# Performance work log

Measured on AMD Instinct MI355X. Metric: run time of the kernel, lower is better.

## Reference

```python
import jax, jax.numpy as jnp
from jax import lax
import numpy as np

S, B, I, H, O = 65536, 1, 2, 128, 1


def setup_inputs() -> dict:
    key = jax.random.key(0)
    k1, k2, k3, k4 = jax.random.split(key, 4)
    # xavier_normal-style scales
    s_ih = (2.0 / (4 * H + I)) ** 0.5
    s_hh = (2.0 / (4 * H + H)) ** 0.5
    s_out = (2.0 / (H + O)) ** 0.5
    return {
        "x": jax.random.normal(k1, (S, B, I), jnp.float32),
        "h0": jnp.zeros((1, B, H), jnp.float32),
        "c0": jnp.zeros((1, B, H), jnp.float32),
        "W_ih": jax.random.normal(k2, (4 * H, I), jnp.float32) * s_ih,
        "W_hh": jax.random.normal(k3, (4 * H, H), jnp.float32) * s_hh,
        "b_ih": jnp.zeros((4 * H,), jnp.float32),
        "b_hh": jnp.zeros((4 * H,), jnp.float32),
        "W_out": jax.random.normal(k4, (O, H), jnp.float32) * s_out,
        "b_out": jnp.zeros((O,), jnp.float32),
    }


def reference(x, h0, c0, W_ih, W_hh, b_ih, b_hh, W_out, b_out):
    # Precompute input-to-gate projections for all timesteps: (S, B, 4H)
    xg = jnp.einsum("sbi,gi->sbg", x, W_ih) + b_ih + b_hh

    def step(carry, xg_t):
        h, c = carry  # (B, H) each
        gates = xg_t + h @ W_hh.T  # (B, 4H); PyTorch order i,f,g,o
        i, f, g, o = jnp.split(gates, 4, axis=-1)
        i = jax.nn.sigmoid(i)
        f = jax.nn.sigmoid(f)
        g = jnp.tanh(g)
        o = jax.nn.sigmoid(o)
        c = f * c + i * g
        h = o * jnp.tanh(c)
        return (h, c), h

    (_, _), hs = lax.scan(step, (h0[0], c0[0]), xg)  # hs: (S, B, H)
    out = jnp.tanh(hs.transpose(1, 0, 2))  # (B, S, H), matches permute(1,0,2)
    out = out @ W_out.T + b_out  # (B, S, O)
    return out.reshape(out.shape[0] * out.shape[1], -1)  # (B*S, O)
```

## Files before the change

kernel.cpp:

```cpp
#include <hip/hip_runtime.h>

#define S_LEN 65536
#define HDIM 128
#define NTHR 1024

typedef _Float16 half2_t __attribute__((ext_vector_type(2)));
typedef _Float16 half8_t __attribute__((ext_vector_type(8)));

__device__ __forceinline__ float sigm(float x) {
    return 1.0f / (1.0f + __expf(-x));
}
__device__ __forceinline__ float tanh_fast(float x) {
    return 2.0f / (1.0f + __expf(-2.0f * x)) - 1.0f;
}

__device__ __forceinline__ float dot2(half2_t a, half2_t b, float c) {
#if __has_builtin(__builtin_amdgcn_fdot2)
    return __builtin_amdgcn_fdot2(a, b, c, false);
#else
    return fmaf((float)a.x, (float)b.x, fmaf((float)a.y, (float)b.y, c));
#endif
}

#define H_HI_OFF 144

__global__ __launch_bounds__(NTHR)
__attribute__((amdgpu_waves_per_eu(4, 4)))
void lstm_seq_h(const float* __restrict__ x,
                const float* __restrict__ h0,
                const float* __restrict__ c0,
                const float* __restrict__ W_ih,
                const float* __restrict__ W_hh,
                const float* __restrict__ b_ih,
                const float* __restrict__ b_hh,
                _Float16* __restrict__ h_hist)
{
    __shared__ __align__(16) unsigned char h_raw[2 * H_HI_OFF];
    __shared__ float gates_part[2 * 512];

    const int tid  = threadIdx.x;
    const int j    = tid >> 1;
    const int half = tid & 1;

    const float2* wr2 = (const float2*)(W_hh + j * HDIM + half * 64);
#define WDEF(i) half2_t W##i; { float2 t = wr2[i]; \
        W##i.x = (_Float16)t.x; W##i.y = (_Float16)t.y; } \
        asm volatile("" : "+v"(W##i));
    WDEF(0)  WDEF(1)  WDEF(2)  WDEF(3)  WDEF(4)  WDEF(5)  WDEF(6)  WDEF(7)
    WDEF(8)  WDEF(9)  WDEF(10) WDEF(11) WDEF(12) WDEF(13) WDEF(14) WDEF(15)
    WDEF(16) WDEF(17) WDEF(18) WDEF(19) WDEF(20) WDEF(21) WDEF(22) WDEF(23)
    WDEF(24) WDEF(25) WDEF(26) WDEF(27) WDEF(28) WDEF(29) WDEF(30) WDEF(31)
#undef WDEF

    float wih0 = 0.0f, wih1 = 0.0f, bias = 0.0f;
    if (half == 0) {
        wih0 = W_ih[2 * j + 0];
        wih1 = W_ih[2 * j + 1];
        bias = b_ih[j] + b_hh[j];
    }

    float c = 0.0f;
    _Float16* hw = (_Float16*)(h_raw + ((tid < 64) ? 2 * tid
                                                   : H_HI_OFF + 2 * (tid - 64)));
    if (tid < HDIM) {
        c = c0[tid];
        *hw = (_Float16)h0[tid];
    }
    __syncthreads();

    const float2* xp = (const float2*)x;
    float2 xcur = xp[0];
    const half8_t* hp = (const half8_t*)(h_raw + half * H_HI_OFF);

    #pragma unroll 1
    for (int t = 0; t < S_LEN; ++t) {
        const int tn = (t + 1 < S_LEN) ? (t + 1) : (S_LEN - 1);
        float2 xnext = xp[tn];

        float a0 = fmaf(wih0, xcur.x, fmaf(wih1, xcur.y, bias));
        float a1 = 0.0f, a2 = 0.0f, a3 = 0.0f;

#define CHUNK(cc, w0_, w1_, w2_, w3_) {                         \
        half8_t hv = hp[cc];                                    \
        half2_t p0 = { hv[0], hv[1] };                          \
        half2_t p1 = { hv[2], hv[3] };                          \
        half2_t p2 = { hv[4], hv[5] };                          \
        half2_t p3 = { hv[6], hv[7] };                          \
        a0 = dot2(w0_, p0, a0);                                 \
        a1 = dot2(w1_, p1, a1);                                 \
        a2 = dot2(w2_, p2, a2);                                 \
        a3 = dot2(w3_, p3, a3); }
        CHUNK(0, W0,  W1,  W2,  W3)
        CHUNK(1, W4,  W5,  W6,  W7)
        CHUNK(2, W8,  W9,  W10, W11)
        CHUNK(3, W12, W13, W14, W15)
        CHUNK(4, W16, W17, W18, W19)
        CHUNK(5, W20, W21, W22, W23)
        CHUNK(6, W24, W25, W26, W27)
        CHUNK(7, W28, W29, W30, W31)
#undef CHUNK

        gates_part[half * 512 + j] = (a0 + a1) + (a2 + a3);
        __syncthreads();

        if (tid < HDIM) {
            float gi = sigm(gates_part[tid]           + gates_part[tid + 512]);
            float gf = sigm(gates_part[tid + 128]     + gates_part[tid + 640]);
            float gg = tanh_fast(gates_part[tid + 256] + gates_part[tid + 768]);
            float go = sigm(gates_part[tid + 384]     + gates_part[tid + 896]);
            c = fmaf(gf, c, gi * gg);
            float h = go * tanh_fast(c);
            _Float16 hf = (_Float16)h;
            *hw = hf;
            h_hist[t * HDIM + tid] = hf;
        }
        __syncthreads();

        xcur = xnext;
    }
}

__global__ __launch_bounds__(256)
void out_proj(const _Float16* __restrict__ h_hist,
              const float* __restrict__ W_out,
              const float* __restrict__ b_out,
              float* __restrict__ out)
{
    const int lane  = threadIdx.x & 63;
    const int gwave = (blockIdx.x * 256 + threadIdx.x) >> 6;
    const int nwave = (gridDim.x * 256) >> 6;

    const float wo0 = W_out[2 * lane + 0];
    const float wo1 = W_out[2 * lane + 1];
    const float bout = b_out[0];

    for (int t = gwave; t < S_LEN; t += nwave) {
        half2_t hv = ((const half2_t*)(h_hist + t * HDIM))[lane];
        float p = tanh_fast((float)hv.x) * wo0 + tanh_fast((float)hv.y) * wo1;
        #pragma unroll
        for (int off = 32; off > 0; off >>= 1)
            p += __shfl_xor(p, off, 64);
        if (lane == 0) out[t] = p + bout;
    }
}

__global__ __launch_bounds__(NTHR)
__attribute__((amdgpu_waves_per_eu(4, 4)))
void lstm_seq_full(const float* __restrict__ x,
                   const float* __restrict__ h0,
                   const float* __restrict__ c0,
                   const float* __restrict__ W_ih,
                   const float* __restrict__ W_hh,
                   const float* __restrict__ b_ih,
                   const float* __restrict__ b_hh,
                   const float* __restrict__ W_out,
                   const float* __restrict__ b_out,
                   float* __restrict__ out)
{
    __shared__ __align__(16) unsigned char h_raw[2 * H_HI_OFF];
    __shared__ float gates_part[2 * 512];
    __shared__ float red_sh[2];

    const int tid  = threadIdx.x;
    const int j    = tid >> 1;
    const int half = tid & 1;

    const float2* wr2 = (const float2*)(W_hh + j * HDIM + half * 64);
#define WDEF(i) half2_t W##i; { float2 t = wr2[i]; \
        W##i.x = (_Float16)t.x; W##i.y = (_Float16)t.y; } \
        asm volatile("" : "+v"(W##i));
    WDEF(0)  WDEF(1)  WDEF(2)  WDEF(3)  WDEF(4)  WDEF(5)  WDEF(6)  WDEF(7)
    WDEF(8)  WDEF(9)  WDEF(10) WDEF(11) WDEF(12) WDEF(13) WDEF(14) WDEF(15)
    WDEF(16) WDEF(17) WDEF(18) WDEF(19) WDEF(20) WDEF(21) WDEF(22) WDEF(23)
    WDEF(24) WDEF(25) WDEF(26) WDEF(27) WDEF(28) WDEF(29) WDEF(30) WDEF(31)
#undef WDEF

    float wih0 = 0.0f, wih1 = 0.0f, bias = 0.0f;
    if (half == 0) {
        wih0 = W_ih[2 * j + 0];
        wih1 = W_ih[2 * j + 1];
        bias = b_ih[j] + b_hh[j];
    }

    float c = 0.0f, wout = 0.0f;
    _Float16* hw = (_Float16*)(h_raw + ((tid < 64) ? 2 * tid
                                                   : H_HI_OFF + 2 * (tid - 64)));
    if (tid < HDIM) {
        c = c0[tid];
        wout = W_out[tid];
        *hw = (_Float16)h0[tid];
    }
    const float bout = b_out[0];
    __syncthreads();

    const float2* xp = (const float2*)x;
    float2 xcur = xp[0];
    const half8_t* hp = (const half8_t*)(h_raw + half * H_HI_OFF);

    #pragma unroll 1
    for (int t = 0; t < S_LEN; ++t) {
        const int tn = (t + 1 < S_LEN) ? (t + 1) : (S_LEN - 1);
        float2 xnext = xp[tn];

        float a0 = fmaf(wih0, xcur.x, fmaf(wih1, xcur.y, bias));
        float a1 = 0.0f, a2 = 0.0f, a3 = 0.0f;

#define CHUNK(cc, w0_, w1_, w2_, w3_) {                         \
        half8_t hv = hp[cc];                                    \
        half2_t p0 = { hv[0], hv[1] };                          \
        half2_t p1 = { hv[2], hv[3] };                          \
        half2_t p2 = { hv[4], hv[5] };                          \
        half2_t p3 = { hv[6], hv[7] };                          \
        a0 = dot2(w0_, p0, a0);                                 \
        a1 = dot2(w1_, p1, a1);                                 \
        a2 = dot2(w2_, p2, a2);                                 \
        a3 = dot2(w3_, p3, a3); }
        CHUNK(0, W0,  W1,  W2,  W3)
        CHUNK(1, W4,  W5,  W6,  W7)
        CHUNK(2, W8,  W9,  W10, W11)
        CHUNK(3, W12, W13, W14, W15)
        CHUNK(4, W16, W17, W18, W19)
        CHUNK(5, W20, W21, W22, W23)
        CHUNK(6, W24, W25, W26, W27)
        CHUNK(7, W28, W29, W30, W31)
#undef CHUNK

        gates_part[half * 512 + j] = (a0 + a1) + (a2 + a3);
        __syncthreads();

        if (tid < HDIM) {
            float gi = sigm(gates_part[tid]           + gates_part[tid + 512]);
            float gf = sigm(gates_part[tid + 128]     + gates_part[tid + 640]);
            float gg = tanh_fast(gates_part[tid + 256] + gates_part[tid + 768]);
            float go = sigm(gates_part[tid + 384]     + gates_part[tid + 896]);
            c = fmaf(gf, c, gi * gg);
            float h = go * tanh_fast(c);
            *hw = (_Float16)h;

            float p = tanh_fast(h) * wout;
            #pragma unroll
            for (int off = 32; off > 0; off >>= 1)
                p += __shfl_xor(p, off, 64);
            if ((tid & 63) == 0) red_sh[tid >> 6] = p;
        }
        __syncthreads();

        if (tid == 0) out[t] = red_sh[0] + red_sh[1] + bout;
        xcur = xnext;
    }
}

extern "C" void kernel_launch(void* const* d_in, const int* in_sizes, int n_in,
                              void* d_out, int out_size, void* d_ws, size_t ws_size,
                              hipStream_t stream) {
    const float* x     = (const float*)d_in[0];
    const float* h0    = (const float*)d_in[1];
    const float* c0    = (const float*)d_in[2];
    const float* W_ih  = (const float*)d_in[3];
    const float* W_hh  = (const float*)d_in[4];
    const float* b_ih  = (const float*)d_in[5];
    const float* b_hh  = (const float*)d_in[6];
    const float* W_out = (const float*)d_in[7];
    const float* b_out = (const float*)d_in[8];

    const size_t need = (size_t)S_LEN * HDIM * sizeof(_Float16);
    if (ws_size >= need) {
        _Float16* h_hist = (_Float16*)d_ws;
        lstm_seq_h<<<dim3(1), dim3(NTHR), 0, stream>>>(
            x, h0, c0, W_ih, W_hh, b_ih, b_hh, h_hist);
        out_proj<<<dim3(1024), dim3(256), 0, stream>>>(
            h_hist, W_out, b_out, (float*)d_out);
    } else {
        lstm_seq_full<<<dim3(1), dim3(NTHR), 0, stream>>>(
            x, h0, c0, W_ih, W_hh, b_ih, b_hh, W_out, b_out, (float*)d_out);
    }
}
```

Baseline: 45.95 ms.

## Compute recurrent gate matvec with MFMA 16x16x32 in a 512-thread block

Result: faster. 44.20 ms (-3.8%).

```diff
diff --git a/kernel.cpp b/kernel.cpp
--- a/kernel.cpp
+++ b/kernel.cpp
@@ -2,10 +2,10 @@
 
 #define S_LEN 65536
 #define HDIM 128
-#define NTHR 1024
 
 typedef _Float16 half2_t __attribute__((ext_vector_type(2)));
 typedef _Float16 half8_t __attribute__((ext_vector_type(8)));
+typedef float f32x4 __attribute__((ext_vector_type(4)));
 
 __device__ __forceinline__ float sigm(float x) {
     return 1.0f / (1.0f + __expf(-x));
@@ -13,7 +13,6 @@
 __device__ __forceinline__ float tanh_fast(float x) {
     return 2.0f / (1.0f + __expf(-2.0f * x)) - 1.0f;
 }
-
 __device__ __forceinline__ float dot2(half2_t a, half2_t b, float c) {
 #if __has_builtin(__builtin_amdgcn_fdot2)
     return __builtin_amdgcn_fdot2(a, b, c, false);
@@ -22,21 +21,161 @@
 #endif
 }
 
+__global__ __launch_bounds__(512)
+__attribute__((amdgpu_waves_per_eu(2, 2)))
+void lstm_seq_mfma(const float* __restrict__ x,
+                   const float* __restrict__ h0,
+                   const float* __restrict__ c0,
+                   const float* __restrict__ W_ih,
+                   const float* __restrict__ W_hh,
+                   const float* __restrict__ b_ih,
+                   const float* __restrict__ b_hh,
+                   _Float16* __restrict__ h_hist)
+{
+    __shared__ __align__(16) _Float16 h_sh16[HDIM];
+    __shared__ __align__(16) float gates_sh[4 * HDIM];
+
+    const int tid  = threadIdx.x;
+    const int lane = tid & 63;
+    const int w    = tid >> 6;
+    const int m    = lane & 15;
+    const int quad = lane >> 4;
+
+#define LOAD_AF(i, q) \
+    half8_t af_##i##_##q; { \
+        const float* s_ = W_hh + (size_t)(w * 64 + 16 * (i) + m) * HDIM \
+                               + 32 * (q) + 8 * quad; \
+        af_##i##_##q = (half8_t){ \
+            (_Float16)s_[0], (_Float16)s_[1], (_Float16)s_[2], (_Float16)s_[3], \
+            (_Float16)s_[4], (_Float16)s_[5], (_Float16)s_[6], (_Float16)s_[7] }; \
+        asm volatile("" : "+v"(af_##i##_##q)); }
+    LOAD_AF(0, 0) LOAD_AF(0, 1) LOAD_AF(0, 2) LOAD_AF(0, 3)
+    LOAD_AF(1, 0) LOAD_AF(1, 1) LOAD_AF(1, 2) LOAD_AF(1, 3)
+    LOAD_AF(2, 0) LOAD_AF(2, 1) LOAD_AF(2, 2) LOAD_AF(2, 3)
+    LOAD_AF(3, 0) LOAD_AF(3, 1) LOAD_AF(3, 2) LOAD_AF(3, 3)
+#undef LOAD_AF
+
+    float wi0x = 0.f, wi0y = 0.f, bs0 = 0.f;
+    float wi1x = 0.f, wi1y = 0.f, bs1 = 0.f;
+    float wi2x = 0.f, wi2y = 0.f, bs2 = 0.f;
+    float wi3x = 0.f, wi3y = 0.f, bs3 = 0.f;
+    float c = 0.0f;
+    if (tid < HDIM) {
+        wi0x = W_ih[2 * tid];            wi0y = W_ih[2 * tid + 1];
+        wi1x = W_ih[2 * (tid + 128)];    wi1y = W_ih[2 * (tid + 128) + 1];
+        wi2x = W_ih[2 * (tid + 256)];    wi2y = W_ih[2 * (tid + 256) + 1];
+        wi3x = W_ih[2 * (tid + 384)];    wi3y = W_ih[2 * (tid + 384) + 1];
+        bs0 = b_ih[tid]       + b_hh[tid];
+        bs1 = b_ih[tid + 128] + b_hh[tid + 128];
+        bs2 = b_ih[tid + 256] + b_hh[tid + 256];
+        bs3 = b_ih[tid + 384] + b_hh[tid + 384];
+        c = c0[tid];
+        h_sh16[tid] = (_Float16)h0[tid];
+    }
+    __syncthreads();
+
+    const float2* xp = (const float2*)x;
+    float2 xcur = {0.f, 0.f}, xnext = {0.f, 0.f};
+    if (tid < HDIM) xcur = xp[0];
+
+    half8_t bf0 = (half8_t){0,0,0,0,0,0,0,0};
+    half8_t bf1 = bf0, bf2 = bf0, bf3 = bf0;
+
+    #pragma unroll 1
+    for (int t = 0; t < S_LEN; ++t) {
+        if (m == 0) {
+            const half8_t* hb = (const half8_t*)h_sh16;
+            bf0 = hb[quad];
+            bf1 = hb[4 + quad];
+            bf2 = hb[8 + quad];
+            bf3 = hb[12 + quad];
+        }
+        f32x4 acc0 = {0.f, 0.f, 0.f, 0.f};
+        f32x4 acc1 = {0.f, 0.f, 0.f, 0.f};
+        f32x4 acc2 = {0.f, 0.f, 0.f, 0.f};
+        f32x4 acc3 = {0.f, 0.f, 0.f, 0.f};
+#define MFMA_TILE(i) \
+        acc##i = __builtin_amdgcn_mfma_f32_16x16x32_f16(af_##i##_0, bf0, acc##i, 0, 0, 0); \
+        acc##i = __builtin_amdgcn_mfma_f32_16x16x32_f16(af_##i##_1, bf1, acc##i, 0, 0, 0); \
+        acc##i = __builtin_amdgcn_mfma_f32_16x16x32_f16(af_##i##_2, bf2, acc##i, 0, 0, 0); \
+        acc##i = __builtin_amdgcn_mfma_f32_16x16x32_f16(af_##i##_3, bf3, acc##i, 0, 0, 0);
+        MFMA_TILE(0) MFMA_TILE(1) MFMA_TILE(2) MFMA_TILE(3)
+#undef MFMA_TILE
+        if (m == 0) {
+            f32x4* gp = (f32x4*)gates_sh + w * 16 + quad;
+            gp[0]  = acc0;
+            gp[4]  = acc1;
+            gp[8]  = acc2;
+            gp[12] = acc3;
+        }
+
+        if (tid < HDIM) {
+            const int tn = (t + 1 < S_LEN) ? (t + 1) : (S_LEN - 1);
+            xnext = xp[tn];
+        }
+        __syncthreads();
+
+        if (tid < HDIM) {
+            float gi = sigm(gates_sh[tid]
+                            + fmaf(wi0x, xcur.x, fmaf(wi0y, xcur.y, bs0)));
+            float gf = sigm(gates_sh[tid + 128]
+                            + fmaf(wi1x, xcur.x, fmaf(wi1y, xcur.y, bs1)));
+            float gg = tanh_fast(gates_sh[tid + 256]
+                            + fmaf(wi2x, xcur.x, fmaf(wi2y, xcur.y, bs2)));
+            float go = sigm(gates_sh[tid + 384]
+                            + fmaf(wi3x, xcur.x, fmaf(wi3y, xcur.y, bs3)));
+            c = fmaf(gf, c, gi * gg);
+            float h = go * tanh_fast(c);
+            _Float16 hf = (_Float16)h;
+            h_sh16[tid] = hf;
+            h_hist[t * HDIM + tid] = hf;
+            xcur = xnext;
+        }
+        __syncthreads();
+    }
+}
+
+__global__ __launch_bounds__(256)
+void out_proj(const _Float16* __restrict__ h_hist,
+              const float* __restrict__ W_out,
+              const float* __restrict__ b_out,
+              float* __restrict__ out)
+{
+    const int lane  = threadIdx.x & 63;
+    const int gwave = (blockIdx.x * 256 + threadIdx.x) >> 6;
+    const int nwave = (gridDim.x * 256) >> 6;
+
+    const float wo0 = W_out[2 * lane + 0];
+    const float wo1 = W_out[2 * lane + 1];
+    const float bout = b_out[0];
+
+    for (int t = gwave; t < S_LEN; t += nwave) {
+        half2_t hv = ((const half2_t*)(h_hist + t * HDIM))[lane];
+        float p = tanh_fast((float)hv.x) * wo0 + tanh_fast((float)hv.y) * wo1;
+        #pragma unroll
+        for (int off = 32; off > 0; off >>= 1)
+            p += __shfl_xor(p, off, 64);
+        if (lane == 0) out[t] = p + bout;
+    }
+}
+
 #define H_HI_OFF 144
-
-__global__ __launch_bounds__(NTHR)
+__global__ __launch_bounds__(1024)
 __attribute__((amdgpu_waves_per_eu(4, 4)))
-void lstm_seq_h(const float* __restrict__ x,
-                const float* __restrict__ h0,
-                const float* __restrict__ c0,
-                const float* __restrict__ W_ih,
-                const float* __restrict__ W_hh,
-                const float* __restrict__ b_ih,
-                const float* __restrict__ b_hh,
-                _Float16* __restrict__ h_hist)
+void lstm_seq_full(const float* __restrict__ x,
+                   const float* __restrict__ h0,
+                   const float* __restrict__ c0,
+                   const float* __restrict__ W_ih,
+                   const float* __restrict__ W_hh,
+                   const float* __restrict__ b_ih,
+                   const float* __restrict__ b_hh,
+                   const float* __restrict__ W_out,
+                   const float* __restrict__ b_out,
+                   float* __restrict__ out)
 {
     __shared__ __align__(16) unsigned char h_raw[2 * H_HI_OFF];
     __shared__ float gates_part[2 * 512];
+    __shared__ float red_sh[2];
 
     const int tid  = threadIdx.x;
     const int j    = tid >> 1;
@@ -59,13 +198,15 @@
         bias = b_ih[j] + b_hh[j];
     }
 
-    float c = 0.0f;
+    float c = 0.0f, wout = 0.0f;
     _Float16* hw = (_Float16*)(h_raw + ((tid < 64) ? 2 * tid
                                                    : H_HI_OFF + 2 * (tid - 64)));
     if (tid < HDIM) {
         c = c0[tid];
+        wout = W_out[tid];
         *hw = (_Float16)h0[tid];
     }
+    const float bout = b_out[0];
     __syncthreads();
 
     const float2* xp = (const float2*)x;
@@ -104,135 +245,10 @@
         __syncthreads();
 
         if (tid < HDIM) {
-            float gi = sigm(gates_part[tid]           + gates_part[tid + 512]);
-            float gf = sigm(gates_part[tid + 128]     + gates_part[tid + 640]);
+            float gi = sigm(gates_part[tid]            + gates_part[tid + 512]);
+            float gf = sigm(gates_part[tid + 128]      + gates_part[tid + 640]);
             float gg = tanh_fast(gates_part[tid + 256] + gates_part[tid + 768]);
-            float go = sigm(gates_part[tid + 384]     + gates_part[tid + 896]);
-            c = fmaf(gf, c, gi * gg);
-            float h = go * tanh_fast(c);
-            _Float16 hf = (_Float16)h;
-            *hw = hf;
-            h_hist[t * HDIM + tid] = hf;
-        }
-        __syncthreads();
-
-        xcur = xnext;
-    }
-}
-
-__global__ __launch_bounds__(256)
-void out_proj(const _Float16* __restrict__ h_hist,
-              const float* __restrict__ W_out,
-              const float* __restrict__ b_out,
-              float* __restrict__ out)
-{
-    const int lane  = threadIdx.x & 63;
-    const int gwave = (blockIdx.x * 256 + threadIdx.x) >> 6;
-    const int nwave = (gridDim.x * 256) >> 6;
-
-    const float wo0 = W_out[2 * lane + 0];
-    const float wo1 = W_out[2 * lane + 1];
-    const float bout = b_out[0];
-
-    for (int t = gwave; t < S_LEN; t += nwave) {
-        half2_t hv = ((const half2_t*)(h_hist + t * HDIM))[lane];
-        float p = tanh_fast((float)hv.x) * wo0 + tanh_fast((float)hv.y) * wo1;
-        #pragma unroll
-        for (int off = 32; off > 0; off >>= 1)
-            p += __shfl_xor(p, off, 64);
-        if (lane == 0) out[t] = p + bout;
-    }
-}
-
-__global__ __launch_bounds__(NTHR)
-__attribute__((amdgpu_waves_per_eu(4, 4)))
-void lstm_seq_full(const float* __restrict__ x,
-                   const float* __restrict__ h0,
-                   const float* __restrict__ c0,
-                   const float* __restrict__ W_ih,
-                   const float* __restrict__ W_hh,
-                   const float* __restrict__ b_ih,
-                   const float* __restrict__ b_hh,
-                   const float* __restrict__ W_out,
-                   const float* __restrict__ b_out,
-                   float* __restrict__ out)
-{
-    __shared__ __align__(16) unsigned char h_raw[2 * H_HI_OFF];
-    __shared__ float gates_part[2 * 512];
-    __shared__ float red_sh[2];
-
-    const int tid  = threadIdx.x;
-    const int j    = tid >> 1;
-    const int half = tid & 1;
-
-    const float2* wr2 = (const float2*)(W_hh + j * HDIM + half * 64);
-#define WDEF(i) half2_t W##i; { float2 t = wr2[i]; \
-        W##i.x = (_Float16)t.x; W##i.y = (_Float16)t.y; } \
-        asm volatile("" : "+v"(W##i));
-    WDEF(0)  WDEF(1)  WDEF(2)  WDEF(3)  WDEF(4)  WDEF(5)  WDEF(6)  WDEF(7)
-    WDEF(8)  WDEF(9)  WDEF(10) WDEF(11) WDEF(12) WDEF(13) WDEF(14) WDEF(15)
-    WDEF(16) WDEF(17) WDEF(18) WDEF(19) WDEF(20) WDEF(21) WDEF(22) WDEF(23)
-    WDEF(24) WDEF(25) WDEF(26) WDEF(27) WDEF(28) WDEF(29) WDEF(30) WDEF(31)
-#undef WDEF
-
-    float wih0 = 0.0f, wih1 = 0.0f, bias = 0.0f;
-    if (half == 0) {
-        wih0 = W_ih[2 * j + 0];
-        wih1 = W_ih[2 * j + 1];
-        bias = b_ih[j] + b_hh[j];
-    }
-
-    float c = 0.0f, wout = 0.0f;
-    _Float16* hw = (_Float16*)(h_raw + ((tid < 64) ? 2 * tid
-                                                   : H_HI_OFF + 2 * (tid - 64)));
-    if (tid < HDIM) {
-        c = c0[tid];
-        wout = W_out[tid];
-        *hw = (_Float16)h0[tid];
-    }
-    const float bout = b_out[0];
-    __syncthreads();
-
-    const float2* xp = (const float2*)x;
-    float2 xcur = xp[0];
-    const half8_t* hp = (const half8_t*)(h_raw + half * H_HI_OFF);
-
-    #pragma unroll 1
-    for (int t = 0; t < S_LEN; ++t) {
-        const int tn = (t + 1 < S_LEN) ? (t + 1) : (S_LEN - 1);
-        float2 xnext = xp[tn];
-
-        float a0 = fmaf(wih0, xcur.x, fmaf(wih1, xcur.y, bias));
-        float a1 = 0.0f, a2 = 0.0f, a3 = 0.0f;
-
-#define CHUNK(cc, w0_, w1_, w2_, w3_) {                         \
-        half8_t hv = hp[cc];                                    \
-        half2_t p0 = { hv[0], hv[1] };                          \
-        half2_t p1 = { hv[2], hv[3] };                          \
-        half2_t p2 = { hv[4], hv[5] };                          \
-        half2_t p3 = { hv[6], hv[7] };                          \
-        a0 = dot2(w0_, p0, a0);                                 \
-        a1 = dot2(w1_, p1, a1);                                 \
-        a2 = dot2(w2_, p2, a2);                                 \
-        a3 = dot2(w3_, p3, a3); }
-        CHUNK(0, W0,  W1,  W2,  W3)
-        CHUNK(1, W4,  W5,  W6,  W7)
-        CHUNK(2, W8,  W9,  W10, W11)
-        CHUNK(3, W12, W13, W14, W15)
-        CHUNK(4, W16, W17, W18, W19)
-        CHUNK(5, W20, W21, W22, W23)
-        CHUNK(6, W24, W25, W26, W27)
-        CHUNK(7, W28, W29, W30, W31)
-#undef CHUNK
-
-        gates_part[half * 512 + j] = (a0 + a1) + (a2 + a3);
-        __syncthreads();
-
-        if (tid < HDIM) {
-            float gi = sigm(gates_part[tid]           + gates_part[tid + 512]);
-            float gf = sigm(gates_part[tid + 128]     + gates_part[tid + 640]);
-            float gg = tanh_fast(gates_part[tid + 256] + gates_part[tid + 768]);
-            float go = sigm(gates_part[tid + 384]     + gates_part[tid + 896]);
+            float go = sigm(gates_part[tid + 384]      + gates_part[tid + 896]);
             c = fmaf(gf, c, gi * gg);
             float h = go * tanh_fast(c);
             *hw = (_Float16)h;
@@ -266,12 +282,12 @@
     const size_t need = (size_t)S_LEN * HDIM * sizeof(_Float16);
     if (ws_size >= need) {
         _Float16* h_hist = (_Float16*)d_ws;
-        lstm_seq_h<<<dim3(1), dim3(NTHR), 0, stream>>>(
+        lstm_seq_mfma<<<dim3(1), dim3(512), 0, stream>>>(
             x, h0, c0, W_ih, W_hh, b_ih, b_hh, h_hist);
         out_proj<<<dim3(1024), dim3(256), 0, stream>>>(
             h_hist, W_out, b_out, (float*)d_out);
     } else {
-        lstm_seq_full<<<dim3(1), dim3(NTHR), 0, stream>>>(
+        lstm_seq_full<<<dim3(1), dim3(1024), 0, stream>>>(
             x, h0, c0, W_ih, W_hh, b_ih, b_hh, W_out, b_out, (float*)d_out);
     }
 }
```
